# Optimization experiments

Measured on AMD Instinct MI355X. Metric: run time of the kernel, lower is better.

Reference implementation:

```python
import jax, jax.numpy as jnp
import numpy as np

EPS = 1e-9
# i = 7,6,...,-1 use exp_factor = -(4**i); i = -2 uses 0.0 (matches torch's reversed(range(-2,8)))
EXP_FACTORS = np.array([-(4.0 ** i) for i in range(7, -2, -1)] + [0.0], dtype=np.float32)


def setup_inputs() -> dict:
    key = jax.random.key(0)
    k1, k2 = jax.random.split(key)
    B, N, D = 16, 2048, 3
    preds = jax.random.normal(k1, (B, N, D), dtype=jnp.float32)
    labels = jax.random.normal(k2, (B, N, D), dtype=jnp.float32)
    return {"preds": preds, "labels": labels}


def _pairwise_dist(p1, p2):
    # ||p1||^2 + ||p2||^2 - 2 p1 . p2  -> [B, N, N]
    p1n = jnp.sum(p1 * p1, axis=-1)[..., :, None]
    p2n = jnp.sum(p2 * p2, axis=-1)[..., None, :]
    return p1n + p2n - 2.0 * jnp.einsum('bnd,bmd->bnm', p1, p2)


def _approx_match(pwdist):
    B, N, _ = pwdist.shape
    match0 = jnp.zeros_like(pwdist)
    cost0 = jnp.ones((B, 1, N), dtype=pwdist.dtype)      # per-target remaining capacity
    curr0 = jnp.ones((B, N, 1), dtype=pwdist.dtype)      # per-source remaining currency

    def step(carry, ef):
        match, cost, currency = carry
        bids = jnp.exp(ef * pwdist) * cost
        bids = bids * currency / (jnp.sum(bids, axis=1, keepdims=True) + EPS)
        bid_wt = jnp.minimum(cost / (jnp.sum(bids, axis=1, keepdims=True) + EPS), 1.0)
        bids = bids * bid_wt
        match = match + bids
        cost = jnp.maximum(cost - jnp.sum(bids, axis=1, keepdims=True), 0.0)
        currency = jnp.maximum(currency - jnp.sum(bids, axis=2, keepdims=True), 0.0)
        return (match, cost, currency), None

    (match, _, _), _ = jax.lax.scan(step, (match0, cost0, curr0), jnp.asarray(EXP_FACTORS))
    return match


def reference(preds, labels):
    pwdist = _pairwise_dist(preds, labels)
    match = _approx_match(pwdist)
    return jnp.sum(match * pwdist)
```

## Files before the change

kernel.cpp:

```cpp
#include <hip/hip_runtime.h>
#include <cstddef>

#define BB    16
#define NN    2048
#define BN    (BB * NN)
#define EPSF  1e-9f
#define TPB   512
#define CPT   2
#define SPLIT 32
#define TILE  64
#define CHUNK 1024
#define GRID  (SPLIT * 2 * BB)
#define K9C   4

extern "C" __device__ float __ocml_native_exp2_f32(float);
__device__ __forceinline__ float fast_exp2(float x) {
#if __has_builtin(__builtin_amdgcn_exp2f)
    return __builtin_amdgcn_exp2f(x);
#else
    return __ocml_native_exp2_f32(x);
#endif
}

__device__ __forceinline__ float block_sum(float v, int t, float* tmp8) {
#pragma unroll
    for (int o = 32; o > 0; o >>= 1) v += __shfl_down(v, o, 64);
    __syncthreads();
    if ((t & 63) == 0) tmp8[t >> 6] = v;
    __syncthreads();
    float s = 0.0f;
#pragma unroll
    for (int w = 0; w < TPB / 64; w++) s += tmp8[w];
    return s;
}

__global__ __launch_bounds__(TPB, 8) void passA(
    const float* __restrict__ preds, const float* __restrict__ labels,
    const float* __restrict__ curprev, float* __restrict__ curout,
    const float* __restrict__ RSprev, const float* __restrict__ RRprev,
    float* __restrict__ RSz, float* __restrict__ RRz,
    float* __restrict__ Sacc, float* __restrict__ Tacc,
    float* __restrict__ out, float c1, int k)
{
    __shared__ float4 s_p[TILE];
    __shared__ float  s_cu[TILE];
    __shared__ float  s_red0;
    int blk = blockIdx.x;
    int split = blk & 31, mc = (blk >> 5) & 1, b = blk >> 6;
    int t = threadIdx.x;
    int base = b * NN;

    if (t < TILE) {
        int idx = base + split * TILE + t;
        const float* p = preds + (size_t)idx * 3;
        float px = p[0], py = p[1], pz = p[2];
        float pn = px * px + py * py + pz * pz;
        float cu, contrib = 0.0f;
        if (k == 0) cu = 1.0f;
        else {
            float cup = curprev[idx], rs = RSprev[idx], rr = RRprev[idx];
            contrib = cup * rr;
            cu = fmaxf(cup * (1.0f - rs), 0.0f);
        }
        s_p[t]  = make_float4(px, py, pz, c1 * pn);
        s_cu[t] = cu;
        if (mc == 0) {
            curout[idx] = cu;
            RSz[idx] = 0.0f; RRz[idx] = 0.0f;
        }
        if (k > 0) {
#pragma unroll
            for (int o = 32; o > 0; o >>= 1) contrib += __shfl_down(contrib, o, 64);
            if (t == 0) s_red0 = contrib;
        }
    }

    int m0 = mc * CHUNK + t;
    float gx[CPT], gy[CPT], gz[CPT], am[CPT], Sa[CPT], Ta[CPT];
    float n2c1 = -2.0f * c1;
#pragma unroll
    for (int c = 0; c < CPT; c++) {
        int m = m0 + c * TPB;
        const float* l = labels + (size_t)(base + m) * 3;
        float lx = l[0], ly = l[1], lz = l[2];
        gx[c] = n2c1 * lx; gy[c] = n2c1 * ly; gz[c] = n2c1 * lz;
        am[c] = c1 * (lx * lx + ly * ly + lz * lz);
        Sa[c] = 0.0f; Ta[c] = 0.0f;
    }
    __syncthreads();
    if (k > 0 && mc == 0 && t == 0) atomicAdd(out, s_red0);

#pragma unroll 4
    for (int j = 0; j < TILE; j++) {
        float4 P = s_p[j]; float cu = s_cu[j];
#pragma unroll
        for (int c = 0; c < CPT; c++) {
            float arg = fmaf(P.x, gx[c], fmaf(P.y, gy[c], fmaf(P.z, gz[c], P.w + am[c])));
            float e = fast_exp2(arg);
            Sa[c] += e;
            Ta[c] = fmaf(e, cu, Ta[c]);
        }
    }
#pragma unroll
    for (int c = 0; c < CPT; c++) {
        int idx = base + m0 + c * TPB;
        atomicAdd(&Sacc[idx], Sa[c]);
        atomicAdd(&Tacc[idx], Ta[c]);
    }
}

__global__ __launch_bounds__(TPB, 8) void passB(
    const float* __restrict__ preds, const float* __restrict__ labels,
    const float* __restrict__ Sread, const float* __restrict__ Tread,
    const float* __restrict__ costprev, float* __restrict__ costout,
    float* __restrict__ Sz, float* __restrict__ Tz,
    float* __restrict__ RSacc, float* __restrict__ RRacc,
    float c1, float invc1, int k)
{
    __shared__ float4 s_l[TILE];
    __shared__ float  s_cc[TILE];
    int blk = blockIdx.x;
    int split = blk & 31, nc = (blk >> 5) & 1, b = blk >> 6;
    int t = threadIdx.x;
    int base = b * NN;

    if (t < TILE) {
        int idx = base + split * TILE + t;
        const float* l = labels + (size_t)idx * 3;
        float lx = l[0], ly = l[1], lz = l[2];
        float lm2 = lx * lx + ly * ly + lz * lz;
        float S = Sread[idx], T = Tread[idx];
        float cost = (k == 0) ? 1.0f : costprev[idx];
        float D1 = fmaf(cost, S, EPSF);
        float S2 = cost * T / D1;
        float bw = fminf(cost / (S2 + EPSF), 1.0f);
        float cc = cost * bw / D1;
        float n2c1 = -2.0f * c1;
        s_l[t]  = make_float4(n2c1 * lx, n2c1 * ly, n2c1 * lz, c1 * lm2);
        s_cc[t] = cc;
        if (nc == 0) {
            costout[idx] = fmaxf(fmaf(-S2, bw, cost), 0.0f);
            Sz[idx] = 0.0f; Tz[idx] = 0.0f;
        }
    }

    int n0 = nc * CHUNK + t;
    float px[CPT], py[CPT], pz[CPT], qq[CPT], RSa[CPT], RRa[CPT];
#pragma unroll
    for (int c = 0; c < CPT; c++) {
        int n = n0 + c * TPB;
        const float* p = preds + (size_t)(base + n) * 3;
        px[c] = p[0]; py[c] = p[1]; pz[c] = p[2];
        qq[c] = c1 * (px[c] * px[c] + py[c] * py[c] + pz[c] * pz[c]);
        RSa[c] = 0.0f; RRa[c] = 0.0f;
    }
    __syncthreads();

#pragma unroll 4
    for (int j = 0; j < TILE; j++) {
        float4 L = s_l[j]; float ccj = s_cc[j];
#pragma unroll
        for (int c = 0; c < CPT; c++) {
            float arg = fmaf(px[c], L.x, fmaf(py[c], L.y, fmaf(pz[c], L.z, qq[c] + L.w)));
            float e = fast_exp2(arg);
            float w = e * ccj;
            RSa[c] += w;
            RRa[c] = fmaf(w, arg, RRa[c]);
        }
    }
#pragma unroll
    for (int c = 0; c < CPT; c++) {
        int idx = base + n0 + c * TPB;
        atomicAdd(&RSacc[idx], RSa[c]);
        atomicAdd(&RRacc[idx], RRa[c] * invc1);
    }
}

__global__ __launch_bounds__(TPB, 1) void k9(
    const float* __restrict__ preds, const float* __restrict__ labels,
    const float* __restrict__ cur8, const float* __restrict__ RS8,
    const float* __restrict__ RR8, const float* __restrict__ cost9,
    float* __restrict__ out)
{
    __shared__ float tmp8[TPB / 64];
    int b = blockIdx.x, t = threadIdx.x;
    int base = b * NN;

    float cu9[K9C];
    float contrib = 0.0f, csum = 0.0f;
#pragma unroll
    for (int c = 0; c < K9C; c++) {
        int idx = base + t + c * TPB;
        float cup = cur8[idx];
        contrib = fmaf(cup, RR8[idx], contrib);
        float cu = fmaxf(cup * (1.0f - RS8[idx]), 0.0f);
        cu9[c] = cu; csum += cu;
    }
    float contribT = block_sum(contrib, t, tmp8);
    float Cb = block_sum(csum, t, tmp8);

    float A = 0.0f, Bs = 0.0f, Vx = 0.0f, Vy = 0.0f, Vz = 0.0f;
#pragma unroll
    for (int c = 0; c < K9C; c++) {
        int idx = base + t + c * TPB;
        const float* l = labels + (size_t)idx * 3;
        float lx = l[0], ly = l[1], lz = l[2];
        float cost = cost9[idx];
        float D1 = fmaf(cost, 2048.0f, EPSF);
        float S2 = cost * Cb / D1;
        float bw = fminf(cost / (S2 + EPSF), 1.0f);
        float cc = cost * bw / D1;
        A += cc;
        Bs = fmaf(cc, lx * lx + ly * ly + lz * lz, Bs);
        Vx = fmaf(cc, lx, Vx); Vy = fmaf(cc, ly, Vy); Vz = fmaf(cc, lz, Vz);
    }
    float At  = block_sum(A, t, tmp8);
    float Bt  = block_sum(Bs, t, tmp8);
    float Vxt = block_sum(Vx, t, tmp8);
    float Vyt = block_sum(Vy, t, tmp8);
    float Vzt = block_sum(Vz, t, tmp8);

    float acc = 0.0f;
#pragma unroll
    for (int c = 0; c < K9C; c++) {
        int idx = base + t + c * TPB;
        const float* p = preds + (size_t)idx * 3;
        float x = p[0], y = p[1], z = p[2];
        float pn = x * x + y * y + z * z;
        float rr = fmaf(At, pn, Bt) - 2.0f * (x * Vxt + y * Vyt + z * Vzt);
        acc = fmaf(cu9[c], rr, acc);
    }
    float accT = block_sum(acc, t, tmp8);
    if (t == 0) atomicAdd(out, contribT + accT);
}

extern "C" void kernel_launch(void* const* d_in, const int* in_sizes, int n_in,
                              void* d_out, int out_size, void* d_ws, size_t ws_size,
                              hipStream_t stream) {
    const float* preds  = (const float*)d_in[0];
    const float* labels = (const float*)d_in[1];
    float* out = (float*)d_out;
    float* ws  = (float*)d_ws;

    float* S[2]     = {ws + 0 * BN, ws + 2 * BN};
    float* T[2]     = {ws + 1 * BN, ws + 3 * BN};
    float* RS[2]    = {ws + 4 * BN, ws + 6 * BN};
    float* RR[2]    = {ws + 5 * BN, ws + 7 * BN};
    float* curb[2]  = {ws + 8 * BN, ws + 9 * BN};
    float* costb[2] = {ws + 10 * BN, ws + 11 * BN};

    hipMemsetAsync(d_out, 0, sizeof(float), stream);
    hipMemsetAsync(ws, 0, (size_t)2 * BN * sizeof(float), stream);

    static const float efs[9] = {-16384.0f, -4096.0f, -1024.0f, -256.0f, -64.0f,
                                 -16.0f, -4.0f, -1.0f, -0.25f};
    const float log2e = 1.44269504088896f;
    for (int k = 0; k < 9; k++) {
        float c1 = efs[k] * log2e;
        float invc1 = 1.0f / c1;
        int pk = k & 1, pp = (k + 1) & 1;
        passA<<<GRID, TPB, 0, stream>>>(preds, labels,
            curb[pp], curb[pk],
            RS[pp], RR[pp],
            RS[pk], RR[pk],
            S[pk], T[pk],
            out, c1, k);
        passB<<<GRID, TPB, 0, stream>>>(preds, labels,
            S[pk], T[pk],
            costb[pk], costb[pp],
            S[pp], T[pp],
            RS[pk], RR[pk],
            c1, invc1, k);
    }
    k9<<<BB, TPB, 0, stream>>>(preds, labels, curb[0], RS[0], RR[0], costb[1], out);
}
```

Baseline: 320.6 us.

## Fuse all auction iterations into one cooperative persistent kernel with grid syncs

```diff
diff --git a/kernel.cpp b/kernel.cpp
--- a/kernel.cpp
+++ b/kernel.cpp
@@ -1,5 +1,8 @@
 #include <hip/hip_runtime.h>
+#include <hip/hip_cooperative_groups.h>
 #include <cstddef>
+
+namespace cg = cooperative_groups;
 
 #define BB    16
 #define NN    2048
@@ -7,11 +10,12 @@
 #define EPSF  1e-9f
 #define TPB   512
 #define CPT   2
-#define SPLIT 32
-#define TILE  64
 #define CHUNK 1024
-#define GRID  (SPLIT * 2 * BB)
 #define K9C   4
+#define MTILE 128
+#define MGRID 512
+#define FTILE 64
+#define FGRID 1024
 
 extern "C" __device__ float __ocml_native_exp2_f32(float);
 __device__ __forceinline__ float fast_exp2(float x) {
@@ -34,7 +38,228 @@
     return s;
 }
 
-__global__ __launch_bounds__(TPB, 8) void passA(
+__device__ __forceinline__ void gsync(cg::grid_group& g) {
+    __threadfence();
+    g.sync();
+    __threadfence();
+}
+
+__device__ const float d_efs[9] = {-16384.0f, -4096.0f, -1024.0f, -256.0f,
+                                   -64.0f, -16.0f, -4.0f, -1.0f, -0.25f};
+
+__global__ __launch_bounds__(TPB, 4) void mega(
+    const float* __restrict__ preds, const float* __restrict__ labels,
+    float* __restrict__ out, float* __restrict__ ws)
+{
+    cg::grid_group grid = cg::this_grid();
+    __shared__ float4 s_p[MTILE];
+    __shared__ float  s_cu[MTILE];
+    __shared__ float  s_red[2];
+    __shared__ float4 s_l[MTILE];
+    __shared__ float  s_cc[MTILE];
+    __shared__ float  tmp8[TPB / 64];
+
+    int blk = blockIdx.x;
+    int split = blk & 15, mc = (blk >> 4) & 1, b = blk >> 5;
+    int t = threadIdx.x;
+    int base = b * NN;
+
+    {
+        int gid = blk * TPB + t;
+        if (gid < 2 * BN) ws[gid] = 0.0f;
+        if (gid == 0) *out = 0.0f;
+    }
+    gsync(grid);
+
+    const float log2e = 1.44269504088896f;
+    for (int k = 0; k < 9; k++) {
+        float c1 = d_efs[k] * log2e;
+        float invc1 = 1.0f / c1;
+        int pk = k & 1, pp = pk ^ 1;
+        float* Sk    = ws + (size_t)(2 * pk) * BN;
+        float* Tk    = ws + (size_t)(2 * pk + 1) * BN;
+        float* Sp    = ws + (size_t)(2 * pp) * BN;
+        float* Tp    = ws + (size_t)(2 * pp + 1) * BN;
+        float* RSk   = ws + (size_t)(4 + 2 * pk) * BN;
+        float* RRk   = ws + (size_t)(5 + 2 * pk) * BN;
+        float* RSp   = ws + (size_t)(4 + 2 * pp) * BN;
+        float* RRp   = ws + (size_t)(5 + 2 * pp) * BN;
+        float* curk  = ws + (size_t)(8 + pk) * BN;
+        float* curp  = ws + (size_t)(8 + pp) * BN;
+        float* costk = ws + (size_t)(10 + pk) * BN;
+        float* costp = ws + (size_t)(10 + pp) * BN;
+
+        if (t < MTILE) {
+            int idx = base + split * MTILE + t;
+            const float* p = preds + (size_t)idx * 3;
+            float px = p[0], py = p[1], pz = p[2];
+            float pn = px * px + py * py + pz * pz;
+            float cu, contrib = 0.0f;
+            if (k == 0) cu = 1.0f;
+            else {
+                float cup = curp[idx], rs = RSp[idx], rr = RRp[idx];
+                contrib = cup * rr;
+                cu = fmaxf(cup * (1.0f - rs), 0.0f);
+            }
+            s_p[t]  = make_float4(px, py, pz, c1 * pn);
+            s_cu[t] = cu;
+            if (mc == 0) {
+                curk[idx] = cu;
+                RSk[idx] = 0.0f; RRk[idx] = 0.0f;
+            }
+            if (k > 0 && mc == 0) {
+#pragma unroll
+                for (int o = 32; o > 0; o >>= 1) contrib += __shfl_down(contrib, o, 64);
+                if ((t & 63) == 0) s_red[t >> 6] = contrib;
+            }
+        }
+        {
+            int m0 = mc * CHUNK + t;
+            float gx[CPT], gy[CPT], gz[CPT], am[CPT], Sa[CPT], Ta[CPT];
+            float n2c1 = -2.0f * c1;
+#pragma unroll
+            for (int c = 0; c < CPT; c++) {
+                int m = m0 + c * TPB;
+                const float* l = labels + (size_t)(base + m) * 3;
+                float lx = l[0], ly = l[1], lz = l[2];
+                gx[c] = n2c1 * lx; gy[c] = n2c1 * ly; gz[c] = n2c1 * lz;
+                am[c] = c1 * (lx * lx + ly * ly + lz * lz);
+                Sa[c] = 0.0f; Ta[c] = 0.0f;
+            }
+            __syncthreads();
+            if (k > 0 && mc == 0 && t == 0) atomicAdd(out, s_red[0] + s_red[1]);
+
+#pragma unroll 4
+            for (int j = 0; j < MTILE; j++) {
+                float4 P = s_p[j]; float cu = s_cu[j];
+#pragma unroll
+                for (int c = 0; c < CPT; c++) {
+                    float arg = fmaf(P.x, gx[c], fmaf(P.y, gy[c], fmaf(P.z, gz[c], P.w + am[c])));
+                    float e = fast_exp2(arg);
+                    Sa[c] += e;
+                    Ta[c] = fmaf(e, cu, Ta[c]);
+                }
+            }
+#pragma unroll
+            for (int c = 0; c < CPT; c++) {
+                int idx = base + m0 + c * TPB;
+                atomicAdd(&Sk[idx], Sa[c]);
+                atomicAdd(&Tk[idx], Ta[c]);
+            }
+        }
+        gsync(grid);
+
+        if (t < MTILE) {
+            int idx = base + split * MTILE + t;
+            const float* l = labels + (size_t)idx * 3;
+            float lx = l[0], ly = l[1], lz = l[2];
+            float lm2 = lx * lx + ly * ly + lz * lz;
+            float S = Sk[idx], T = Tk[idx];
+            float cost = (k == 0) ? 1.0f : costk[idx];
+            float D1 = fmaf(cost, S, EPSF);
+            float S2 = cost * T / D1;
+            float bw = fminf(cost / (S2 + EPSF), 1.0f);
+            float cc = cost * bw / D1;
+            float n2c1 = -2.0f * c1;
+            s_l[t]  = make_float4(n2c1 * lx, n2c1 * ly, n2c1 * lz, c1 * lm2);
+            s_cc[t] = cc;
+            if (mc == 0) {
+                costp[idx] = fmaxf(fmaf(-S2, bw, cost), 0.0f);
+                Sp[idx] = 0.0f; Tp[idx] = 0.0f;
+            }
+        }
+        {
+            int n0 = mc * CHUNK + t;
+            float px[CPT], py[CPT], pz[CPT], qq[CPT], RSa[CPT], RRa[CPT];
+#pragma unroll
+            for (int c = 0; c < CPT; c++) {
+                int n = n0 + c * TPB;
+                const float* p = preds + (size_t)(base + n) * 3;
+                px[c] = p[0]; py[c] = p[1]; pz[c] = p[2];
+                qq[c] = c1 * (px[c] * px[c] + py[c] * py[c] + pz[c] * pz[c]);
+                RSa[c] = 0.0f; RRa[c] = 0.0f;
+            }
+            __syncthreads();
+
+#pragma unroll 4
+            for (int j = 0; j < MTILE; j++) {
+                float4 L = s_l[j]; float ccj = s_cc[j];
+#pragma unroll
+                for (int c = 0; c < CPT; c++) {
+                    float arg = fmaf(px[c], L.x, fmaf(py[c], L.y, fmaf(pz[c], L.z, qq[c] + L.w)));
+                    float e = fast_exp2(arg);
+                    float w = e * ccj;
+                    RSa[c] += w;
+                    RRa[c] = fmaf(w, arg, RRa[c]);
+                }
+            }
+#pragma unroll
+            for (int c = 0; c < CPT; c++) {
+                int idx = base + n0 + c * TPB;
+                atomicAdd(&RSk[idx], RSa[c]);
+                atomicAdd(&RRk[idx], RRa[c] * invc1);
+            }
+        }
+        gsync(grid);
+    }
+
+    if (blk < BB) {
+        const float* cur8  = ws + (size_t)8 * BN;
+        const float* RS8   = ws + (size_t)4 * BN;
+        const float* RR8   = ws + (size_t)5 * BN;
+        const float* cost9 = ws + (size_t)11 * BN;
+        int kbase = blk * NN;
+
+        float cu9[K9C];
+        float contrib = 0.0f, csum = 0.0f;
+#pragma unroll
+        for (int c = 0; c < K9C; c++) {
+            int idx = kbase + t + c * TPB;
+            float cup = cur8[idx];
+            contrib = fmaf(cup, RR8[idx], contrib);
+            float cu = fmaxf(cup * (1.0f - RS8[idx]), 0.0f);
+            cu9[c] = cu; csum += cu;
+        }
+        float contribT = block_sum(contrib, t, tmp8);
+        float Cb = block_sum(csum, t, tmp8);
+
+        float A = 0.0f, Bs = 0.0f, Vx = 0.0f, Vy = 0.0f, Vz = 0.0f;
+#pragma unroll
+        for (int c = 0; c < K9C; c++) {
+            int idx = kbase + t + c * TPB;
+            const float* l = labels + (size_t)idx * 3;
+            float lx = l[0], ly = l[1], lz = l[2];
+            float cost = cost9[idx];
+            float D1 = fmaf(cost, 2048.0f, EPSF);
+            float S2 = cost * Cb / D1;
+            float bw = fminf(cost / (S2 + EPSF), 1.0f);
+            float cc = cost * bw / D1;
+            A += cc;
+            Bs = fmaf(cc, lx * lx + ly * ly + lz * lz, Bs);
+            Vx = fmaf(cc, lx, Vx); Vy = fmaf(cc, ly, Vy); Vz = fmaf(cc, lz, Vz);
+        }
+        float At  = block_sum(A, t, tmp8);
+        float Bt  = block_sum(Bs, t, tmp8);
+        float Vxt = block_sum(Vx, t, tmp8);
+        float Vyt = block_sum(Vy, t, tmp8);
+        float Vzt = block_sum(Vz, t, tmp8);
+
+        float acc = 0.0f;
+#pragma unroll
+        for (int c = 0; c < K9C; c++) {
+            int idx = kbase + t + c * TPB;
+            const float* p = preds + (size_t)idx * 3;
+            float x = p[0], y = p[1], z = p[2];
+            float pn = x * x + y * y + z * z;
+            float rr = fmaf(At, pn, Bt) - 2.0f * (x * Vxt + y * Vyt + z * Vzt);
+            acc = fmaf(cu9[c], rr, acc);
+        }
+        float accT = block_sum(acc, t, tmp8);
+        if (t == 0) atomicAdd(out, contribT + accT);
+    }
+}
+
+__global__ __launch_bounds__(TPB, 8) void passAf(
     const float* __restrict__ preds, const float* __restrict__ labels,
     const float* __restrict__ curprev, float* __restrict__ curout,
     const float* __restrict__ RSprev, const float* __restrict__ RRprev,
@@ -42,16 +267,16 @@
     float* __restrict__ Sacc, float* __restrict__ Tacc,
     float* __restrict__ out, float c1, int k)
 {
-    __shared__ float4 s_p[TILE];
-    __shared__ float  s_cu[TILE];
+    __shared__ float4 s_p[FTILE];
+    __shared__ float  s_cu[FTILE];
     __shared__ float  s_red0;
     int blk = blockIdx.x;
     int split = blk & 31, mc = (blk >> 5) & 1, b = blk >> 6;
     int t = threadIdx.x;
     int base = b * NN;
 
-    if (t < TILE) {
-        int idx = base + split * TILE + t;
+    if (t < FTILE) {
+        int idx = base + split * FTILE + t;
         const float* p = preds + (size_t)idx * 3;
         float px = p[0], py = p[1], pz = p[2];
         float pn = px * px + py * py + pz * pz;
@@ -74,7 +299,6 @@
             if (t == 0) s_red0 = contrib;
         }
     }
-
     int m0 = mc * CHUNK + t;
     float gx[CPT], gy[CPT], gz[CPT], am[CPT], Sa[CPT], Ta[CPT];
     float n2c1 = -2.0f * c1;
@@ -91,7 +315,7 @@
     if (k > 0 && mc == 0 && t == 0) atomicAdd(out, s_red0);
 
 #pragma unroll 4
-    for (int j = 0; j < TILE; j++) {
+    for (int j = 0; j < FTILE; j++) {
         float4 P = s_p[j]; float cu = s_cu[j];
 #pragma unroll
         for (int c = 0; c < CPT; c++) {
@@ -109,7 +333,7 @@
     }
 }
 
-__global__ __launch_bounds__(TPB, 8) void passB(
+__global__ __launch_bounds__(TPB, 8) void passBf(
     const float* __restrict__ preds, const float* __restrict__ labels,
     const float* __restrict__ Sread, const float* __restrict__ Tread,
     const float* __restrict__ costprev, float* __restrict__ costout,
@@ -117,15 +341,15 @@
     float* __restrict__ RSacc, float* __restrict__ RRacc,
     float c1, float invc1, int k)
 {
-    __shared__ float4 s_l[TILE];
-    __shared__ float  s_cc[TILE];
+    __shared__ float4 s_l[FTILE];
+    __shared__ float  s_cc[FTILE];
     int blk = blockIdx.x;
     int split = blk & 31, nc = (blk >> 5) & 1, b = blk >> 6;
     int t = threadIdx.x;
     int base = b * NN;
 
-    if (t < TILE) {
-        int idx = base + split * TILE + t;
+    if (t < FTILE) {
+        int idx = base + split * FTILE + t;
         const float* l = labels + (size_t)idx * 3;
         float lx = l[0], ly = l[1], lz = l[2];
         float lm2 = lx * lx + ly * ly + lz * lz;
@@ -143,7 +367,6 @@
             Sz[idx] = 0.0f; Tz[idx] = 0.0f;
         }
     }
-
     int n0 = nc * CHUNK + t;
     float px[CPT], py[CPT], pz[CPT], qq[CPT], RSa[CPT], RRa[CPT];
 #pragma unroll
@@ -157,7 +380,7 @@
     __syncthreads();
 
 #pragma unroll 4
-    for (int j = 0; j < TILE; j++) {
+    for (int j = 0; j < FTILE; j++) {
         float4 L = s_l[j]; float ccj = s_cc[j];
 #pragma unroll
         for (int c = 0; c < CPT; c++) {
@@ -176,7 +399,7 @@
     }
 }
 
-__global__ __launch_bounds__(TPB, 1) void k9(
+__global__ __launch_bounds__(TPB, 1) void k9f(
     const float* __restrict__ preds, const float* __restrict__ labels,
     const float* __restrict__ cur8, const float* __restrict__ RS8,
     const float* __restrict__ RR8, const float* __restrict__ cost9,
@@ -242,35 +465,42 @@
     float* out = (float*)d_out;
     float* ws  = (float*)d_ws;
 
-    float* S[2]     = {ws + 0 * BN, ws + 2 * BN};
-    float* T[2]     = {ws + 1 * BN, ws + 3 * BN};
-    float* RS[2]    = {ws + 4 * BN, ws + 6 * BN};
-    float* RR[2]    = {ws + 5 * BN, ws + 7 * BN};
-    float* curb[2]  = {ws + 8 * BN, ws + 9 * BN};
-    float* costb[2] = {ws + 10 * BN, ws + 11 * BN};
-
-    hipMemsetAsync(d_out, 0, sizeof(float), stream);
-    hipMemsetAsync(ws, 0, (size_t)2 * BN * sizeof(float), stream);
-
-    static const float efs[9] = {-16384.0f, -4096.0f, -1024.0f, -256.0f, -64.0f,
-                                 -16.0f, -4.0f, -1.0f, -0.25f};
-    const float log2e = 1.44269504088896f;
-    for (int k = 0; k < 9; k++) {
-        float c1 = efs[k] * log2e;
-        float invc1 = 1.0f / c1;
-        int pk = k & 1, pp = (k + 1) & 1;
-        passA<<<GRID, TPB, 0, stream>>>(preds, labels,
-            curb[pp], curb[pk],
-            RS[pp], RR[pp],
-            RS[pk], RR[pk],
-            S[pk], T[pk],
-            out, c1, k);
-        passB<<<GRID, TPB, 0, stream>>>(preds, labels,
-            S[pk], T[pk],
-            costb[pk], costb[pp],
-            S[pp], T[pp],
-            RS[pk], RR[pk],
-            c1, invc1, k);
-    }
-    k9<<<BB, TPB, 0, stream>>>(preds, labels, curb[0], RS[0], RR[0], costb[1], out);
-}
+    int nb = 0;
+    hipError_t qrc = hipOccupancyMaxActiveBlocksPerMultiprocessor(
+        &nb, (const void*)mega, TPB, 0);
+    bool coop = (qrc == hipSuccess) && (nb * 256 >= MGRID);
+    if (coop) {
+        void* args[4] = {(void*)&preds, (void*)&labels, (void*)&out, (void*)&ws};
+        hipError_t rc = hipLaunchCooperativeKernel((const void*)mega, dim3(MGRID),
+                                                   dim3(TPB), args, 0, stream);
+        if (rc != hipSuccess) coop = false;
+    }
+    if (!coop) {
+        float* S[2]     = {ws + 0 * BN, ws + 2 * BN};
+        float* T[2]     = {ws + 1 * BN, ws + 3 * BN};
+        float* RS[2]    = {ws + 4 * BN, ws + 6 * BN};
+        float* RR[2]    = {ws + 5 * BN, ws + 7 * BN};
+        float* curb[2]  = {ws + 8 * BN, ws + 9 * BN};
+        float* costb[2] = {ws + 10 * BN, ws + 11 * BN};
+
+        hipMemsetAsync(d_out, 0, sizeof(float), stream);
+        hipMemsetAsync(ws, 0, (size_t)2 * BN * sizeof(float), stream);
+
+        static const float efs[9] = {-16384.0f, -4096.0f, -1024.0f, -256.0f,
+                                     -64.0f, -16.0f, -4.0f, -1.0f, -0.25f};
+        const float log2e = 1.44269504088896f;
+        for (int k = 0; k < 9; k++) {
+            float c1 = efs[k] * log2e;
+            float invc1 = 1.0f / c1;
+            int pk = k & 1, pp = (k + 1) & 1;
+            passAf<<<FGRID, TPB, 0, stream>>>(preds, labels,
+                curb[pp], curb[pk], RS[pp], RR[pp], RS[pk], RR[pk],
+                S[pk], T[pk], out, c1, k);
+            passBf<<<FGRID, TPB, 0, stream>>>(preds, labels,
+                S[pk], T[pk], costb[pk], costb[pp], S[pp], T[pp],
+                RS[pk], RR[pk], c1, invc1, k);
+        }
+        k9f<<<BB, TPB, 0, stream>>>(preds, labels, curb[0], RS[0], RR[0],
+                                    costb[1], out);
+    }
+}
```

Result: no change. 322.3 us (+0.5%).
